# Performance work log

Hardware: AMD Instinct MI355X
Metric: run time of the kernel (lower is better)

Reference implementation:

```python
import jax, jax.numpy as jnp
import numpy as np

TOP_K = 2

def setup_inputs() -> dict:
    key = jax.random.key(0)
    k1, k2 = jax.random.split(key)
    D, E = 4096, 64
    hidden_states = jax.random.normal(k1, (2, 8192, D), dtype=jnp.float32)
    W = jax.random.normal(k2, (E, D), dtype=jnp.float32) / np.sqrt(D)
    b = jnp.zeros((E,), dtype=jnp.float32)
    return {"hidden_states": hidden_states, "W": W, "b": b}

def reference(hidden_states, W, b):
    # gate: logits [B, S, E]
    logits = jnp.einsum('bsd,ed->bse', hidden_states, W) + b
    scores = jax.nn.softmax(logits, axis=-1)
    top_k_values, top_k_indices = jax.lax.top_k(scores, TOP_K)
    return ((top_k_indices, top_k_values), scores)
```

## Files before the change

kernel.cpp:

```cpp
#include <hip/hip_runtime.h>
#include <math.h>

#define D_DIM 4096
#define E_DIM 64
#define TM 64
#define KSPLIT 4
#define KPART (D_DIM / KSPLIT)
#define CHK 64
#define NCH (KPART / CHK)
#define WROW 72

typedef __attribute__((ext_vector_type(8))) short bf16x8;
typedef __attribute__((ext_vector_type(4))) float f32x4;

__device__ inline void split3(const f32x4 a0, const f32x4 a1,
                              bf16x8& fh, bf16x8& fm, bf16x8& fl) {
    uint uh[8], um[8], ul[8];
    float f[8] = {a0[0], a0[1], a0[2], a0[3], a1[0], a1[1], a1[2], a1[3]};
    #pragma unroll
    for (int j = 0; j < 8; ++j) {
        const uint u = __float_as_uint(f[j]);
        const uint h = u & 0xFFFF0000u;
        const float r = f[j] - __uint_as_float(h);
        const uint m = __float_as_uint(r) & 0xFFFF0000u;
        const float r2 = r - __uint_as_float(m);
        uh[j] = h; um[j] = m; ul[j] = __float_as_uint(r2);
    }
    union { bf16x8 v; uint u[4]; } H, M, L;
    #pragma unroll
    for (int j = 0; j < 4; ++j) {
        H.u[j] = (uh[2*j] >> 16) | (uh[2*j+1] & 0xFFFF0000u);
        M.u[j] = (um[2*j] >> 16) | (um[2*j+1] & 0xFFFF0000u);
        L.u[j] = (ul[2*j] >> 16) | (ul[2*j+1] & 0xFFFF0000u);
    }
    fh = H.v; fm = M.v; fl = L.v;
}

__global__ __launch_bounds__(256, 4) void router_gemm(
    const float* __restrict__ hs,
    const float* __restrict__ W,
    float* __restrict__ logits,
    int nTok)
{
    __shared__ short wsh[E_DIM * WROW];
    __shared__ short wsm[E_DIM * WROW];
    __shared__ short wsl[E_DIM * WROW];

    const int tid  = threadIdx.x;
    const int lane = tid & 63;
    const int wv   = tid >> 6;
    const int part = blockIdx.x & (KSPLIT - 1);
    const int tb   = (blockIdx.x >> 2) * TM;
    const int kb   = part * KPART;

    const int l15 = lane & 15;
    const int lq  = lane >> 4;

    const float* aptr = hs + (size_t)(tb + wv * 16 + l15) * D_DIM + kb + lq * 8;
    const int we = tid >> 2;
    const int wq = tid & 3;
    const float* wptr = W + (size_t)we * D_DIM + kb + wq * 16;

    f32x4 acc[4];
    #pragma unroll
    for (int t = 0; t < 4; ++t) acc[t] = (f32x4){0.f, 0.f, 0.f, 0.f};

    f32x4 ca[4], pa[4], wr[4];

    auto loadA = [&](int ch, f32x4* dst) {
        const float* p = aptr + ch * CHK;
        dst[0] = *(const f32x4*)(p);
        dst[1] = *(const f32x4*)(p + 4);
        dst[2] = *(const f32x4*)(p + 32);
        dst[3] = *(const f32x4*)(p + 36);
    };
    auto loadW = [&](int ch) {
        const float* p = wptr + ch * CHK;
        wr[0] = *(const f32x4*)(p);
        wr[1] = *(const f32x4*)(p + 4);
        wr[2] = *(const f32x4*)(p + 8);
        wr[3] = *(const f32x4*)(p + 12);
    };
    auto storeW = [&]() {
        bf16x8 h0, m0, l0, h1, m1, l1;
        split3(wr[0], wr[1], h0, m0, l0);
        split3(wr[2], wr[3], h1, m1, l1);
        const int base = we * WROW + wq * 16;
        *(bf16x8*)&wsh[base] = h0;  *(bf16x8*)&wsh[base + 8] = h1;
        *(bf16x8*)&wsm[base] = m0;  *(bf16x8*)&wsm[base + 8] = m1;
        *(bf16x8*)&wsl[base] = l0;  *(bf16x8*)&wsl[base + 8] = l1;
    };
    auto compute = [&](const f32x4* a) {
        #pragma unroll
        for (int s = 0; s < 2; ++s) {
            bf16x8 ah, am, al;
            split3(a[2 * s], a[2 * s + 1], ah, am, al);
            const int koff = s * 32 + lq * 8;
            #pragma unroll
            for (int t = 0; t < 4; ++t) {
                const int rb = (t * 16 + l15) * WROW + koff;
                const bf16x8 bh = *(const bf16x8*)&wsh[rb];
                const bf16x8 bm = *(const bf16x8*)&wsm[rb];
                const bf16x8 bl = *(const bf16x8*)&wsl[rb];
                acc[t] = __builtin_amdgcn_mfma_f32_16x16x32_bf16(ah, bh, acc[t], 0, 0, 0);
                acc[t] = __builtin_amdgcn_mfma_f32_16x16x32_bf16(ah, bm, acc[t], 0, 0, 0);
                acc[t] = __builtin_amdgcn_mfma_f32_16x16x32_bf16(am, bh, acc[t], 0, 0, 0);
                acc[t] = __builtin_amdgcn_mfma_f32_16x16x32_bf16(ah, bl, acc[t], 0, 0, 0);
                acc[t] = __builtin_amdgcn_mfma_f32_16x16x32_bf16(al, bh, acc[t], 0, 0, 0);
                acc[t] = __builtin_amdgcn_mfma_f32_16x16x32_bf16(am, bm, acc[t], 0, 0, 0);
            }
        }
    };

    loadA(0, ca);
    loadW(0);
    storeW();
    __syncthreads();
    #pragma unroll 1
    for (int ch = 0; ch < NCH; ++ch) {
        const bool last = (ch == NCH - 1);
        if (!last) loadA(ch + 1, pa);
        compute(ca);
        if (!last) {
            loadW(ch + 1);
            __syncthreads();
            storeW();
            __syncthreads();
            #pragma unroll
            for (int i = 0; i < 4; ++i) ca[i] = pa[i];
        }
    }

    float* dst = logits + (size_t)(tb + wv * 16) * E_DIM;
    #pragma unroll
    for (int t = 0; t < 4; ++t)
        #pragma unroll
        for (int r = 0; r < 4; ++r)
            unsafeAtomicAdd(&dst[(size_t)(lq * 4 + r) * E_DIM + t * 16 + l15], acc[t][r]);
}

__global__ __launch_bounds__(256, 4) void router_epilogue(
    const float* __restrict__ bias,
    float* __restrict__ out,
    int nTok)
{
    const int tid = threadIdx.x;
    const int tok = blockIdx.x * 64 + (tid >> 2);
    const int g   = tid & 3;

    float* out_idx = out;
    float* out_val = out + (size_t)nTok * 2;
    float* sc      = out + (size_t)nTok * 4;

    float* src = sc + (size_t)tok * E_DIM + g * 16;
    float v[16];
    #pragma unroll
    for (int j = 0; j < 4; ++j) {
        const f32x4 x = *(const f32x4*)(src + j * 4);
        const f32x4 b = *(const f32x4*)(bias + g * 16 + j * 4);
        v[j * 4 + 0] = x[0] + b[0];
        v[j * 4 + 1] = x[1] + b[1];
        v[j * 4 + 2] = x[2] + b[2];
        v[j * 4 + 3] = x[3] + b[3];
    }

    float b1 = -INFINITY, b2 = -INFINITY;
    int i1 = 0, i2 = 0;
    #pragma unroll
    for (int j = 0; j < 16; ++j) {
        const float x = v[j];
        const int idx = g * 16 + j;
        if (x > b1)      { b2 = b1; i2 = i1; b1 = x; i1 = idx; }
        else if (x > b2) { b2 = x; i2 = idx; }
    }
    #pragma unroll
    for (int d = 1; d <= 2; d <<= 1) {
        const float ob1 = __shfl_xor(b1, d);
        const int   oi1 = __shfl_xor(i1, d);
        const float ob2 = __shfl_xor(b2, d);
        const int   oi2 = __shfl_xor(i2, d);
        if (ob1 > b1 || (ob1 == b1 && oi1 < i1)) {
            if (b1 > ob2 || (b1 == ob2 && i1 < oi2)) { b2 = b1; i2 = i1; }
            else                                     { b2 = ob2; i2 = oi2; }
            b1 = ob1; i1 = oi1;
        } else {
            if (ob1 > b2 || (ob1 == b2 && oi1 < i2)) { b2 = ob1; i2 = oi1; }
        }
    }
    const float m = b1;

    float e[16];
    float s = 0.f;
    #pragma unroll
    for (int j = 0; j < 16; ++j) { e[j] = __expf(v[j] - m); s += e[j]; }
    s += __shfl_xor(s, 1);
    s += __shfl_xor(s, 2);
    const float inv = 1.f / s;

    if (g == 0) {
        out_idx[(size_t)tok * 2 + 0] = (float)i1;
        out_idx[(size_t)tok * 2 + 1] = (float)i2;
        out_val[(size_t)tok * 2 + 0] = inv;
        out_val[(size_t)tok * 2 + 1] = __expf(b2 - m) * inv;
    }

    #pragma unroll
    for (int j = 0; j < 4; ++j) {
        f32x4 o;
        o[0] = e[j * 4 + 0] * inv;
        o[1] = e[j * 4 + 1] * inv;
        o[2] = e[j * 4 + 2] * inv;
        o[3] = e[j * 4 + 3] * inv;
        *(f32x4*)(src + j * 4) = o;
    }
}

extern "C" void kernel_launch(void* const* d_in, const int* in_sizes, int n_in,
                              void* d_out, int out_size, void* d_ws, size_t ws_size,
                              hipStream_t stream) {
    const float* hs = (const float*)d_in[0];
    const float* W  = (const float*)d_in[1];
    const float* b  = (const float*)d_in[2];
    float* out = (float*)d_out;
    const int nTok = in_sizes[0] / D_DIM;

    float* logits = out + (size_t)nTok * 4;
    hipMemsetAsync(logits, 0, (size_t)nTok * E_DIM * sizeof(float), stream);

    dim3 g1(nTok / TM * KSPLIT), b1(256);
    router_gemm<<<g1, b1, 0, stream>>>(hs, W, logits, nTok);

    dim3 g2(nTok / 64), b2(256);
    router_epilogue<<<g2, b2, 0, stream>>>(b, out, nTok);
}
```

Measured before the change: 384.2 us.

## Switch to scaled fp16 two-way split MFMA with double-buffered weight tiles

Replaces the three-way bf16 split (6 MFMAs per tile) with a two-way fp16 hi/lo split (3 MFMAs per tile), scaling W by 1024 so its low part stays out of the fp16 subnormal range, and unscales at the atomic add. The weight LDS tile is double-buffered, which removes one __syncthreads per chunk, and the W global load is issued before compute. This halves MFMA work and cuts shared-memory traffic, but fp16 has a narrower exponent range, so accuracy depends on activation magnitudes, and round-toward-zero conversion may lose precision.

```diff
diff --git a/kernel.cpp b/kernel.cpp
--- a/kernel.cpp
+++ b/kernel.cpp
@@ -9,31 +9,25 @@
 #define CHK 64
 #define NCH (KPART / CHK)
 #define WROW 72
-
-typedef __attribute__((ext_vector_type(8))) short bf16x8;
+#define WSCALE 1024.0f
+#define ISCALE (1.0f / 1024.0f)
+
+typedef __attribute__((ext_vector_type(8))) __fp16 f16x8;
+typedef __attribute__((ext_vector_type(2))) __fp16 f16x2;
 typedef __attribute__((ext_vector_type(4))) float f32x4;
 
-__device__ inline void split3(const f32x4 a0, const f32x4 a1,
-                              bf16x8& fh, bf16x8& fm, bf16x8& fl) {
-    uint uh[8], um[8], ul[8];
+__device__ inline void split2(const f32x4 a0, const f32x4 a1, f16x8& fh, f16x8& fl) {
     float f[8] = {a0[0], a0[1], a0[2], a0[3], a1[0], a1[1], a1[2], a1[3]};
-    #pragma unroll
-    for (int j = 0; j < 8; ++j) {
-        const uint u = __float_as_uint(f[j]);
-        const uint h = u & 0xFFFF0000u;
-        const float r = f[j] - __uint_as_float(h);
-        const uint m = __float_as_uint(r) & 0xFFFF0000u;
-        const float r2 = r - __uint_as_float(m);
-        uh[j] = h; um[j] = m; ul[j] = __float_as_uint(r2);
-    }
-    union { bf16x8 v; uint u[4]; } H, M, L;
+    union { f16x8 v; f16x2 p[4]; } H, L;
     #pragma unroll
     for (int j = 0; j < 4; ++j) {
-        H.u[j] = (uh[2*j] >> 16) | (uh[2*j+1] & 0xFFFF0000u);
-        M.u[j] = (um[2*j] >> 16) | (um[2*j+1] & 0xFFFF0000u);
-        L.u[j] = (ul[2*j] >> 16) | (ul[2*j+1] & 0xFFFF0000u);
-    }
-    fh = H.v; fm = M.v; fl = L.v;
+        const f16x2 h = __builtin_amdgcn_cvt_pkrtz(f[2*j], f[2*j+1]);
+        const float r0 = f[2*j]     - (float)h[0];
+        const float r1 = f[2*j + 1] - (float)h[1];
+        H.p[j] = h;
+        L.p[j] = __builtin_amdgcn_cvt_pkrtz(r0, r1);
+    }
+    fh = H.v; fl = L.v;
 }
 
 __global__ __launch_bounds__(256, 4) void router_gemm(
@@ -42,9 +36,8 @@
     float* __restrict__ logits,
     int nTok)
 {
-    __shared__ short wsh[E_DIM * WROW];
-    __shared__ short wsm[E_DIM * WROW];
-    __shared__ short wsl[E_DIM * WROW];
+    __shared__ __fp16 wsh[2][E_DIM * WROW];
+    __shared__ __fp16 wsl[2][E_DIM * WROW];
 
     const int tid  = threadIdx.x;
     const int lane = tid & 63;
@@ -81,53 +74,51 @@
         wr[2] = *(const f32x4*)(p + 8);
         wr[3] = *(const f32x4*)(p + 12);
     };
-    auto storeW = [&]() {
-        bf16x8 h0, m0, l0, h1, m1, l1;
-        split3(wr[0], wr[1], h0, m0, l0);
-        split3(wr[2], wr[3], h1, m1, l1);
+    auto storeW = [&](int buf) {
+        f16x8 h0, l0, h1, l1;
+        split2(wr[0] * WSCALE, wr[1] * WSCALE, h0, l0);
+        split2(wr[2] * WSCALE, wr[3] * WSCALE, h1, l1);
         const int base = we * WROW + wq * 16;
-        *(bf16x8*)&wsh[base] = h0;  *(bf16x8*)&wsh[base + 8] = h1;
-        *(bf16x8*)&wsm[base] = m0;  *(bf16x8*)&wsm[base + 8] = m1;
-        *(bf16x8*)&wsl[base] = l0;  *(bf16x8*)&wsl[base + 8] = l1;
-    };
-    auto compute = [&](const f32x4* a) {
+        *(f16x8*)&wsh[buf][base] = h0;  *(f16x8*)&wsh[buf][base + 8] = h1;
+        *(f16x8*)&wsl[buf][base] = l0;  *(f16x8*)&wsl[buf][base + 8] = l1;
+    };
+    auto compute = [&](const f32x4* a, int buf) {
         #pragma unroll
         for (int s = 0; s < 2; ++s) {
-            bf16x8 ah, am, al;
-            split3(a[2 * s], a[2 * s + 1], ah, am, al);
+            f16x8 ah, al;
+            split2(a[2 * s], a[2 * s + 1], ah, al);
             const int koff = s * 32 + lq * 8;
             #pragma unroll
             for (int t = 0; t < 4; ++t) {
                 const int rb = (t * 16 + l15) * WROW + koff;
-                const bf16x8 bh = *(const bf16x8*)&wsh[rb];
-                const bf16x8 bm = *(const bf16x8*)&wsm[rb];
-                const bf16x8 bl = *(const bf16x8*)&wsl[rb];
-                acc[t] = __builtin_amdgcn_mfma_f32_16x16x32_bf16(ah, bh, acc[t], 0, 0, 0);
-                acc[t] = __builtin_amdgcn_mfma_f32_16x16x32_bf16(ah, bm, acc[t], 0, 0, 0);
-                acc[t] = __builtin_amdgcn_mfma_f32_16x16x32_bf16(am, bh, acc[t], 0, 0, 0);
-                acc[t] = __builtin_amdgcn_mfma_f32_16x16x32_bf16(ah, bl, acc[t], 0, 0, 0);
-                acc[t] = __builtin_amdgcn_mfma_f32_16x16x32_bf16(al, bh, acc[t], 0, 0, 0);
-                acc[t] = __builtin_amdgcn_mfma_f32_16x16x32_bf16(am, bm, acc[t], 0, 0, 0);
+                const f16x8 bh = *(const f16x8*)&wsh[buf][rb];
+                const f16x8 bl = *(const f16x8*)&wsl[buf][rb];
+                acc[t] = __builtin_amdgcn_mfma_f32_16x16x32_f16(ah, bh, acc[t], 0, 0, 0);
+                acc[t] = __builtin_amdgcn_mfma_f32_16x16x32_f16(ah, bl, acc[t], 0, 0, 0);
+                acc[t] = __builtin_amdgcn_mfma_f32_16x16x32_f16(al, bh, acc[t], 0, 0, 0);
             }
         }
     };
 
     loadA(0, ca);
     loadW(0);
-    storeW();
+    storeW(0);
     __syncthreads();
+    int buf = 0;
     #pragma unroll 1
     for (int ch = 0; ch < NCH; ++ch) {
         const bool last = (ch == NCH - 1);
-        if (!last) loadA(ch + 1, pa);
-        compute(ca);
         if (!last) {
+            loadA(ch + 1, pa);
             loadW(ch + 1);
-            __syncthreads();
-            storeW();
+        }
+        compute(ca, buf);
+        if (!last) {
+            storeW(buf ^ 1);
             __syncthreads();
             #pragma unroll
             for (int i = 0; i < 4; ++i) ca[i] = pa[i];
+            buf ^= 1;
         }
     }
 
@@ -136,7 +127,7 @@
     for (int t = 0; t < 4; ++t)
         #pragma unroll
         for (int r = 0; r < 4; ++r)
-            unsafeAtomicAdd(&dst[(size_t)(lq * 4 + r) * E_DIM + t * 16 + l15], acc[t][r]);
+            unsafeAtomicAdd(&dst[(size_t)(lq * 4 + r) * E_DIM + t * 16 + l15], acc[t][r] * ISCALE);
 }
 
 __global__ __launch_bounds__(256, 4) void router_epilogue(
```

Result: no change. 382.8 us (-0.4%).
